# Kernel tuning notes

Measured on AMD Instinct MI355X. Metric: run time of the kernel, lower is better.

The kernel has to match this reference:

```python
import jax, jax.numpy as jnp
import numpy as np

NUM_NODE_TYPES = 4
OUT_SHAPE = (3, 3)


def setup_inputs() -> dict:
    key = jax.random.key(0)
    k1, k2, k3, k4 = jax.random.split(key, 4)
    N, E, D = 100000, 1600000, 32
    x = jax.random.normal(k1, (N, D), dtype=jnp.float32)
    edge_index = jax.random.randint(k2, (2, E), 0, N, dtype=jnp.int64)
    node_types = jax.random.randint(k3, (N,), 0, NUM_NODE_TYPES, dtype=jnp.int64)
    # Linear weight: [out_features, in_features] = [prod(out_shape), 2*D + 2*num_node_types]
    W = jax.random.normal(k4, (int(np.prod(OUT_SHAPE)), 2 * D + 2 * NUM_NODE_TYPES), dtype=jnp.float32)
    return {"x": x, "edge_index": edge_index, "node_types": node_types, "W": W}


def reference(x, edge_index, node_types, W):
    src, dst = edge_index[0], edge_index[1]
    # Per-node one-hot type encodings [N, num_node_types]
    nt_oh = jax.nn.one_hot(node_types, NUM_NODE_TYPES, dtype=x.dtype)
    # Gather per-edge features and concat: [E, 2*D + 2*T]
    x_cat = jnp.concatenate([x[src], x[dst], nt_oh[src], nt_oh[dst]], axis=1)
    # Bias-free linear + tanh
    maps = jnp.tanh(jnp.einsum("ef,of->eo", x_cat, W))
    return maps.reshape(-1, OUT_SHAPE[0], OUT_SHAPE[1])
```

## Files before the change

### kernel.cpp

```cpp
#include <hip/hip_runtime.h>
#include <hip/hip_bf16.h>
#include <hip/hip_fp16.h>


#define ODIM 9
#define INF 72
#define ROWB 64
#define TPB 256

__device__ __forceinline__ float fast_tanh(float v) {
    float e = __expf(2.0f * v);
    return 1.0f - 2.0f * __builtin_amdgcn_rcpf(e + 1.0f);
}

__global__ __launch_bounds__(TPB) void node_proj_kernel(
        const float* __restrict__ x, const int* __restrict__ nt,
        const float* __restrict__ W, char* __restrict__ P, int N) {
    int n = blockIdx.x * TPB + threadIdx.x;
    if (n >= N) return;
    float xv[32];
    const float4* xp = (const float4*)(x + (size_t)n * 32);
    #pragma unroll
    for (int i = 0; i < 8; ++i) {
        float4 r = xp[i];
        xv[4*i+0] = r.x; xv[4*i+1] = r.y; xv[4*i+2] = r.z; xv[4*i+3] = r.w;
    }
    int t = nt[n];
    unsigned short hs[10], hd[10];
    #pragma unroll
    for (int o = 0; o < ODIM; ++o) {
        const float* wr = W + o * INF;
        float s1 = wr[64 + t];
        float s2 = wr[68 + t];
        #pragma unroll
        for (int f = 0; f < 32; ++f) {
            s1 += xv[f] * wr[f];
            s2 += xv[f] * wr[32 + f];
        }
        __half h1 = __float2half(s1), h2 = __float2half(s2);
        hs[o] = *(unsigned short*)&h1;
        hd[o] = *(unsigned short*)&h2;
    }
    hs[9] = 0; hd[9] = 0;
    char* row = P + (size_t)n * ROWB;
    union { unsigned short u[8]; uint4 v; } pk;
    #pragma unroll
    for (int i = 0; i < 8; ++i) pk.u[i] = hs[i];
    *(uint4*)(row + 0) = pk.v;
    *(unsigned int*)(row + 16) = (unsigned int)hs[8] | ((unsigned int)hs[9] << 16);
    #pragma unroll
    for (int i = 0; i < 8; ++i) pk.u[i] = hd[i];
    *(uint4*)(row + 32) = pk.v;
    *(unsigned int*)(row + 48) = (unsigned int)hd[8] | ((unsigned int)hd[9] << 16);
}

__device__ __forceinline__ void load9h(const char* p, float* v) {
    uint4 u = *(const uint4*)p;
    unsigned int u2 = *(const unsigned int*)(p + 16);
    const __half2* h = (const __half2*)&u;
    #pragma unroll
    for (int i = 0; i < 4; ++i) {
        float2 f = __half22float2(h[i]);
        v[2*i] = f.x; v[2*i+1] = f.y;
    }
    __half h8 = *(const __half*)&u2;
    v[8] = __half2float(h8);
}

__global__ __launch_bounds__(TPB) void edge_kernel(
        const int* __restrict__ src, const int* __restrict__ dst,
        const char* __restrict__ P, float* __restrict__ out, int E) {
    __shared__ __align__(16) float tile[TPB * ODIM];
    int e0 = blockIdx.x * TPB;
    int cnt = min(TPB, E - e0);
    int e = e0 + (int)threadIdx.x;
    if ((int)threadIdx.x < cnt) {
        int s = src[e];
        int d = dst[e];
        float vs[ODIM], vd[ODIM];
        load9h(P + (size_t)s * ROWB, vs);
        load9h(P + (size_t)d * ROWB + 32, vd);
        #pragma unroll
        for (int k = 0; k < ODIM; ++k)
            tile[threadIdx.x * ODIM + k] = fast_tanh(vs[k] + vd[k]);
    }
    __syncthreads();
    if (cnt == TPB) {
        float4* o4 = (float4*)(out + (size_t)e0 * ODIM);
        const float4* t4 = (const float4*)tile;
        for (int i = threadIdx.x; i < TPB * ODIM / 4; i += TPB)
            o4[i] = t4[i];
    } else {
        for (int i = threadIdx.x; i < cnt * ODIM; i += TPB)
            out[(size_t)e0 * ODIM + i] = tile[i];
    }
}

__global__ __launch_bounds__(TPB) void edge_fused_kernel(
        const int* __restrict__ src, const int* __restrict__ dst,
        const float* __restrict__ x, const int* __restrict__ nt,
        const float* __restrict__ W, float* __restrict__ out, int E) {
    __shared__ __align__(16) float tile[TPB * ODIM];
    int e0 = blockIdx.x * TPB;
    int cnt = min(TPB, E - e0);
    int e = e0 + (int)threadIdx.x;
    if ((int)threadIdx.x < cnt) {
        int s = src[e];
        int d = dst[e];
        float xs[32], xd[32];
        const float4* xsp = (const float4*)(x + (size_t)s * 32);
        const float4* xdp = (const float4*)(x + (size_t)d * 32);
        #pragma unroll
        for (int i = 0; i < 8; ++i) {
            float4 rs = xsp[i], rd = xdp[i];
            xs[4*i+0]=rs.x; xs[4*i+1]=rs.y; xs[4*i+2]=rs.z; xs[4*i+3]=rs.w;
            xd[4*i+0]=rd.x; xd[4*i+1]=rd.y; xd[4*i+2]=rd.z; xd[4*i+3]=rd.w;
        }
        int ts = nt[s], td = nt[d];
        #pragma unroll
        for (int o = 0; o < ODIM; ++o) {
            const float* wr = W + o * INF;
            float acc = wr[64 + ts] + wr[68 + td];
            #pragma unroll
            for (int f = 0; f < 32; ++f)
                acc += xs[f] * wr[f] + xd[f] * wr[32 + f];
            tile[threadIdx.x * ODIM + o] = fast_tanh(acc);
        }
    }
    __syncthreads();
    if (cnt == TPB) {
        float4* o4 = (float4*)(out + (size_t)e0 * ODIM);
        const float4* t4 = (const float4*)tile;
        for (int i = threadIdx.x; i < TPB * ODIM / 4; i += TPB)
            o4[i] = t4[i];
    } else {
        for (int i = threadIdx.x; i < cnt * ODIM; i += TPB)
            out[(size_t)e0 * ODIM + i] = tile[i];
    }
}

extern "C" void kernel_launch(void* const* d_in, const int* in_sizes, int n_in,
                              void* d_out, int out_size, void* d_ws, size_t ws_size,
                              hipStream_t stream) {
    const float* x  = (const float*)d_in[0];
    const int*   ei = (const int*)d_in[1];
    const int*   nt = (const int*)d_in[2];
    const float* W  = (const float*)d_in[3];
    float* out = (float*)d_out;

    int N = in_sizes[2];
    int E = in_sizes[1] / 2;
    const int* src = ei;
    const int* dst = ei + E;

    size_t pbytes = (size_t)N * ROWB;
    if (ws_size >= pbytes) {
        char* P = (char*)d_ws;
        node_proj_kernel<<<(N + TPB - 1) / TPB, TPB, 0, stream>>>(x, nt, W, P, N);
        edge_kernel<<<(E + TPB - 1) / TPB, TPB, 0, stream>>>(src, dst, P, out, E);
    } else {
        edge_fused_kernel<<<(E + TPB - 1) / TPB, TPB, 0, stream>>>(src, dst, x, nt, W, out, E);
    }
}
```

Before: 125.1 us.

## Pack node projections as int16 fixed-point in 36-byte rows with nontemporal I/O

Shrinks each per-node projection row from 64 to 36 bytes by storing the 18 partial sums as int16 fixed-point (scale 512) instead of padded fp16. The node kernel now stages packed rows in shared memory for coalesced vector stores. The edge kernel gathers the row halves with unaligned vector loads and uses nontemporal loads and stores for the edge indices and output. The aim is a smaller gather footprint with better cache line use; the fixed-point range of about ±64 with 1/512 resolution may lose accuracy or saturate large pre-activations.

```diff
diff --git a/kernel.cpp b/kernel.cpp
--- a/kernel.cpp
+++ b/kernel.cpp
@@ -5,8 +5,14 @@
 
 #define ODIM 9
 #define INF 72
-#define ROWB 64
+#define ROWB 36
 #define TPB 256
+#define QSCALE 512.0f
+#define QINV (1.0f / 512.0f)
+
+typedef unsigned int uint4n __attribute__((ext_vector_type(4)));
+typedef unsigned int uint4u __attribute__((ext_vector_type(4), aligned(4)));
+typedef float float4n __attribute__((ext_vector_type(4)));
 
 __device__ __forceinline__ float fast_tanh(float v) {
     float e = __expf(2.0f * v);
@@ -16,55 +22,49 @@
 __global__ __launch_bounds__(TPB) void node_proj_kernel(
         const float* __restrict__ x, const int* __restrict__ nt,
         const float* __restrict__ W, char* __restrict__ P, int N) {
-    int n = blockIdx.x * TPB + threadIdx.x;
-    if (n >= N) return;
-    float xv[32];
-    const float4* xp = (const float4*)(x + (size_t)n * 32);
-    #pragma unroll
-    for (int i = 0; i < 8; ++i) {
-        float4 r = xp[i];
-        xv[4*i+0] = r.x; xv[4*i+1] = r.y; xv[4*i+2] = r.z; xv[4*i+3] = r.w;
+    __shared__ __align__(16) unsigned int stage[TPB * ODIM];
+    int n0 = blockIdx.x * TPB;
+    int cnt = min(TPB, N - n0);
+    int t = (int)threadIdx.x;
+    if (t < cnt) {
+        int n = n0 + t;
+        float xv[32];
+        const float4n* xp = (const float4n*)(x + (size_t)n * 32);
+        #pragma unroll
+        for (int i = 0; i < 8; ++i) {
+            float4n r = __builtin_nontemporal_load(xp + i);
+            xv[4*i+0] = r.x; xv[4*i+1] = r.y; xv[4*i+2] = r.z; xv[4*i+3] = r.w;
+        }
+        int ty = nt[n];
+        short h[18];
+        #pragma unroll
+        for (int o = 0; o < ODIM; ++o) {
+            const float* wr = W + o * INF;
+            float s1 = wr[64 + ty];
+            float s2 = wr[68 + ty];
+            #pragma unroll
+            for (int f = 0; f < 32; ++f) {
+                s1 += xv[f] * wr[f];
+                s2 += xv[f] * wr[32 + f];
+            }
+            h[o]     = (short)__float2int_rn(s1 * QSCALE);
+            h[9 + o] = (short)__float2int_rn(s2 * QSCALE);
+        }
+        #pragma unroll
+        for (int j = 0; j < 9; ++j)
+            stage[t * ODIM + j] = (unsigned int)(unsigned short)h[2*j] |
+                                  ((unsigned int)(unsigned short)h[2*j+1] << 16);
     }
-    int t = nt[n];
-    unsigned short hs[10], hd[10];
-    #pragma unroll
-    for (int o = 0; o < ODIM; ++o) {
-        const float* wr = W + o * INF;
-        float s1 = wr[64 + t];
-        float s2 = wr[68 + t];
-        #pragma unroll
-        for (int f = 0; f < 32; ++f) {
-            s1 += xv[f] * wr[f];
-            s2 += xv[f] * wr[32 + f];
-        }
-        __half h1 = __float2half(s1), h2 = __float2half(s2);
-        hs[o] = *(unsigned short*)&h1;
-        hd[o] = *(unsigned short*)&h2;
+    __syncthreads();
+    char* rowbase = P + (size_t)n0 * ROWB;
+    if (cnt == TPB) {
+        uint4n* o4 = (uint4n*)rowbase;
+        const uint4n* s4 = (const uint4n*)stage;
+        for (int i = t; i < TPB * ODIM / 4; i += TPB) o4[i] = s4[i];
+    } else {
+        unsigned int* o1 = (unsigned int*)rowbase;
+        for (int i = t; i < cnt * ODIM; i += TPB) o1[i] = stage[i];
     }
-    hs[9] = 0; hd[9] = 0;
-    char* row = P + (size_t)n * ROWB;
-    union { unsigned short u[8]; uint4 v; } pk;
-    #pragma unroll
-    for (int i = 0; i < 8; ++i) pk.u[i] = hs[i];
-    *(uint4*)(row + 0) = pk.v;
-    *(unsigned int*)(row + 16) = (unsigned int)hs[8] | ((unsigned int)hs[9] << 16);
-    #pragma unroll
-    for (int i = 0; i < 8; ++i) pk.u[i] = hd[i];
-    *(uint4*)(row + 32) = pk.v;
-    *(unsigned int*)(row + 48) = (unsigned int)hd[8] | ((unsigned int)hd[9] << 16);
-}
-
-__device__ __forceinline__ void load9h(const char* p, float* v) {
-    uint4 u = *(const uint4*)p;
-    unsigned int u2 = *(const unsigned int*)(p + 16);
-    const __half2* h = (const __half2*)&u;
-    #pragma unroll
-    for (int i = 0; i < 4; ++i) {
-        float2 f = __half22float2(h[i]);
-        v[2*i] = f.x; v[2*i+1] = f.y;
-    }
-    __half h8 = *(const __half*)&u2;
-    v[8] = __half2float(h8);
 }
 
 __global__ __launch_bounds__(TPB) void edge_kernel(
@@ -73,25 +73,39 @@
     __shared__ __align__(16) float tile[TPB * ODIM];
     int e0 = blockIdx.x * TPB;
     int cnt = min(TPB, E - e0);
-    int e = e0 + (int)threadIdx.x;
-    if ((int)threadIdx.x < cnt) {
-        int s = src[e];
-        int d = dst[e];
-        float vs[ODIM], vd[ODIM];
-        load9h(P + (size_t)s * ROWB, vs);
-        load9h(P + (size_t)d * ROWB + 32, vd);
+    int t = (int)threadIdx.x;
+    if (t < cnt) {
+        int s = __builtin_nontemporal_load(src + e0 + t);
+        int d = __builtin_nontemporal_load(dst + e0 + t);
+        const char* ps = P + (size_t)s * ROWB;
+        const char* pd = P + (size_t)d * ROWB;
+        uint4u sa = *(const uint4u*)ps;
+        unsigned int sb = *(const unsigned int*)(ps + 16);
+        unsigned int db = *(const unsigned int*)(pd + 16);
+        uint4u da = *(const uint4u*)(pd + 20);
+        int qs[9], qd[9];
+        qs[0]=(short)(sa.x&0xffff); qs[1]=(short)(sa.x>>16);
+        qs[2]=(short)(sa.y&0xffff); qs[3]=(short)(sa.y>>16);
+        qs[4]=(short)(sa.z&0xffff); qs[5]=(short)(sa.z>>16);
+        qs[6]=(short)(sa.w&0xffff); qs[7]=(short)(sa.w>>16);
+        qs[8]=(short)(sb&0xffff);
+        qd[0]=(short)(db>>16);
+        qd[1]=(short)(da.x&0xffff); qd[2]=(short)(da.x>>16);
+        qd[3]=(short)(da.y&0xffff); qd[4]=(short)(da.y>>16);
+        qd[5]=(short)(da.z&0xffff); qd[6]=(short)(da.z>>16);
+        qd[7]=(short)(da.w&0xffff); qd[8]=(short)(da.w>>16);
         #pragma unroll
         for (int k = 0; k < ODIM; ++k)
-            tile[threadIdx.x * ODIM + k] = fast_tanh(vs[k] + vd[k]);
+            tile[t*ODIM + k] = fast_tanh((float)(qs[k] + qd[k]) * QINV);
     }
     __syncthreads();
     if (cnt == TPB) {
-        float4* o4 = (float4*)(out + (size_t)e0 * ODIM);
-        const float4* t4 = (const float4*)tile;
-        for (int i = threadIdx.x; i < TPB * ODIM / 4; i += TPB)
-            o4[i] = t4[i];
+        float4n* o4 = (float4n*)(out + (size_t)e0 * ODIM);
+        const float4n* t4 = (const float4n*)tile;
+        for (int i = t; i < TPB * ODIM / 4; i += TPB)
+            __builtin_nontemporal_store(t4[i], o4 + i);
     } else {
-        for (int i = threadIdx.x; i < cnt * ODIM; i += TPB)
+        for (int i = t; i < cnt * ODIM; i += TPB)
             out[(size_t)e0 * ODIM + i] = tile[i];
     }
 }
@@ -153,8 +167,8 @@
     const int* src = ei;
     const int* dst = ei + E;
 
-    size_t pbytes = (size_t)N * ROWB;
-    if (ws_size >= pbytes) {
+    size_t tbl = (size_t)N * ROWB;
+    if (ws_size >= tbl) {
         char* P = (char*)d_ws;
         node_proj_kernel<<<(N + TPB - 1) / TPB, TPB, 0, stream>>>(x, nt, W, P, N);
         edge_kernel<<<(E + TPB - 1) / TPB, TPB, 0, stream>>>(src, dst, P, out, E);
```

Measured after the change: 119.9 us. 1.04x faster.
